# Performance work log

Measured on AMD Instinct MI355X. Metric: run time of the kernel, lower is better.

Reference implementation:

```python
import jax, jax.numpy as jnp
import numpy as np

N = 50000
E = 800000
IN_DIM = 128
OUT_DIM = 64
NEG_SLOPE = 0.2


def setup_inputs() -> dict:
    key = jax.random.key(0)
    k1, k2, k3, k4, k5 = jax.random.split(key, 5)
    X = jax.random.normal(k1, (N, IN_DIM), dtype=jnp.float32)
    edge_index = jax.random.randint(k2, (2, E), 0, N, dtype=jnp.int64)
    # parameters (xavier-ish scale)
    W = jax.random.normal(k3, (OUT_DIM, IN_DIM), dtype=jnp.float32) * (1.0 / np.sqrt(IN_DIM))
    a_src = jax.random.normal(k4, (OUT_DIM,), dtype=jnp.float32) * 0.1
    a_dst = jax.random.normal(k5, (OUT_DIM,), dtype=jnp.float32) * 0.1
    return {"X": X, "edge_index": edge_index, "num_nodes": N, "W": W, "a_src": a_src, "a_dst": a_dst}


def reference(X, edge_index, num_nodes, W, a_src, a_dst):
    H = X @ W.T                                   # [N, out_dim]
    src, dst = edge_index[0], edge_index[1]       # [E], [E]
    Hs = H[src]                                   # [E, out_dim]
    e = Hs @ a_src + H[dst] @ a_dst               # [E]
    e = jnp.where(e >= 0, e, NEG_SLOPE * e)       # leaky_relu
    e = e - jnp.max(e)                            # global max-shift (as in source)
    exp_e = jnp.exp(e)
    denom = jax.ops.segment_sum(exp_e, dst, num_segments=num_nodes)  # [N]
    alpha = exp_e / (denom[dst] + 1e-12)          # [E]
    weighted = Hs * alpha[:, None]                # [E, out_dim]
    out = jax.ops.segment_sum(weighted, dst, num_segments=num_nodes)  # [N, out_dim]
    return out
```

## Files before the change

### kernel.cpp

```cpp
#include <hip/hip_runtime.h>


#define N_NODES 50000
#define N_EDGES 800000
#define IN_DIM  128
#define OUT_DIM 64
#define NEG_SLOPE 0.2f
#define CAP       64
#define SHARD_W   6250
#define SHRD_BLKS 3200
#define SHRD_EPB  2048

#define WS_H      0
#define WS_SSRC   (N_NODES * OUT_DIM)
#define WS_SDST   (WS_SSRC + N_NODES)
#define WS_COUNT  (WS_SDST + N_NODES)
#define WS_CSR16  (WS_COUNT + N_NODES)

__device__ __forceinline__ int eidx(const void* ei, int use64, long long i) {
    return use64 ? (int)((const long long*)ei)[i] : ((const int*)ei)[i];
}

__global__ __launch_bounds__(256) void gemm_kernel(
        const float* __restrict__ X, const float* __restrict__ W,
        const float* __restrict__ a_src, const float* __restrict__ a_dst,
        float* __restrict__ H, float* __restrict__ s_src, float* __restrict__ s_dst,
        int* __restrict__ count) {
    __shared__ float sWt[IN_DIM][OUT_DIM];
    __shared__ float sX[64][76];
    const int t = threadIdx.x;
    const int row0 = blockIdx.x * 64;
    const int cg = t & 15;
    const int rg = t >> 4;

    if (t < 64 && row0 + t < N_NODES) count[row0 + t] = 0;

    for (int i = t; i < 64 * 32; i += 256) {
        int col = i & 63, k4 = i >> 6;
        float4 w = reinterpret_cast<const float4*>(W)[col * 32 + k4];
        sWt[4 * k4 + 0][col] = w.x;
        sWt[4 * k4 + 1][col] = w.y;
        sWt[4 * k4 + 2][col] = w.z;
        sWt[4 * k4 + 3][col] = w.w;
    }

    float acc[4][4];
    #pragma unroll
    for (int i = 0; i < 4; ++i)
        #pragma unroll
        for (int j = 0; j < 4; ++j) acc[i][j] = 0.f;

    #pragma unroll
    for (int kk = 0; kk < 2; ++kk) {
        const int kb = kk * 64;
        __syncthreads();
        for (int i = t; i < 64 * 16; i += 256) {
            int k4 = i & 15, row = i >> 4;
            int grow = row0 + row;
            float4 x = make_float4(0.f, 0.f, 0.f, 0.f);
            if (grow < N_NODES)
                x = reinterpret_cast<const float4*>(X)[(size_t)grow * 32 + (kb >> 2) + k4];
            sX[4 * k4 + 0][row] = x.x;
            sX[4 * k4 + 1][row] = x.y;
            sX[4 * k4 + 2][row] = x.z;
            sX[4 * k4 + 3][row] = x.w;
        }
        __syncthreads();
        #pragma unroll 4
        for (int k = 0; k < 64; ++k) {
            float4 wv = *reinterpret_cast<const float4*>(&sWt[kb + k][cg * 4]);
            float4 xv = *reinterpret_cast<const float4*>(&sX[k][rg * 4]);
            acc[0][0] += xv.x * wv.x; acc[0][1] += xv.x * wv.y;
            acc[0][2] += xv.x * wv.z; acc[0][3] += xv.x * wv.w;
            acc[1][0] += xv.y * wv.x; acc[1][1] += xv.y * wv.y;
            acc[1][2] += xv.y * wv.z; acc[1][3] += xv.y * wv.w;
            acc[2][0] += xv.z * wv.x; acc[2][1] += xv.z * wv.y;
            acc[2][2] += xv.z * wv.z; acc[2][3] += xv.z * wv.w;
            acc[3][0] += xv.w * wv.x; acc[3][1] += xv.w * wv.y;
            acc[3][2] += xv.w * wv.z; acc[3][3] += xv.w * wv.w;
        }
    }

    float4 as = *reinterpret_cast<const float4*>(&a_src[cg * 4]);
    float4 ad = *reinterpret_cast<const float4*>(&a_dst[cg * 4]);
    #pragma unroll
    for (int i = 0; i < 4; ++i) {
        float ps = acc[i][0] * as.x + acc[i][1] * as.y + acc[i][2] * as.z + acc[i][3] * as.w;
        float pd = acc[i][0] * ad.x + acc[i][1] * ad.y + acc[i][2] * ad.z + acc[i][3] * ad.w;
        #pragma unroll
        for (int off = 1; off < 16; off <<= 1) {
            ps += __shfl_xor(ps, off);
            pd += __shfl_xor(pd, off);
        }
        int row = row0 + rg * 4 + i;
        if (row < N_NODES) {
            *reinterpret_cast<float4*>(&H[(size_t)row * OUT_DIM + cg * 4]) =
                make_float4(acc[i][0], acc[i][1], acc[i][2], acc[i][3]);
            if (cg == 0) { s_src[row] = ps; s_dst[row] = pd; }
        }
    }
}

__global__ __launch_bounds__(256) void scatterfill_kernel(
        const void* __restrict__ ei, int* __restrict__ count,
        unsigned short* __restrict__ csr16) {
    __shared__ int s_use64;
    if (threadIdx.x < 64) {
        unsigned int v = ((const unsigned int*)ei)[2 * threadIdx.x + 1];
        unsigned long long nz = __ballot(v != 0u);
        if (threadIdx.x == 0) s_use64 = (nz == 0ULL) ? 1 : 0;
    }
    __syncthreads();
    const int use64 = s_use64;
    const int shard = blockIdx.x & 7;
    const int bslot = blockIdx.x >> 3;
    const unsigned int dlo = shard * SHARD_W;
    const int base = bslot * SHRD_EPB;
    for (int j = 0; j < SHRD_EPB / 256; ++j) {
        int i = base + j * 256 + threadIdx.x;
        if (i < N_EDGES) {
            unsigned int d = (unsigned int)eidx(ei, use64, (long long)N_EDGES + i);
            if (d - dlo < SHARD_W) {
                int s = eidx(ei, use64, i);
                int pos = atomicAdd(&count[d], 1);
                if (pos < CAP) csr16[((size_t)d << 6) + pos] = (unsigned short)s;
            }
        }
    }
}

__global__ __launch_bounds__(256) void aggregate_kernel(
        const float* __restrict__ H, const float* __restrict__ s_src,
        const float* __restrict__ s_dst, const int* __restrict__ count,
        const unsigned short* __restrict__ csr16, float* __restrict__ out) {
    const int lane = threadIdx.x & 63;
    const int eo   = lane >> 4;
    const int cg   = lane & 15;
    const int dst  = blockIdx.x * 4 + (threadIdx.x >> 6);
    int deg = count[dst];
    deg = (deg < CAP) ? deg : CAP;
    const size_t rs = (size_t)dst << 6;
    const float sd = s_dst[dst];

    int   sl = 0;
    float wl = 0.f;
    if (lane < deg) {
        sl = csr16[rs + lane];
        float tv = s_src[sl] + sd;
        tv = (tv >= 0.f) ? tv : NEG_SLOPE * tv;
        wl = expf(tv);
    }
    float denom = wl;
    #pragma unroll
    for (int off = 32; off; off >>= 1) denom += __shfl_xor(denom, off);

    float4 acc = make_float4(0.f, 0.f, 0.f, 0.f);
    for (int j = 0; j < deg; j += 8) {
        int ja = j + eo, jb = j + 4 + eo;
        float wa = __shfl(wl, ja);
        int   sa = __shfl(sl, ja);
        float wb = __shfl(wl, jb);
        int   sb = __shfl(sl, jb);
        if (ja >= deg) wa = 0.f;
        if (jb >= deg) wb = 0.f;
        float4 ha = *reinterpret_cast<const float4*>(&H[(size_t)sa * OUT_DIM + cg * 4]);
        float4 hb = *reinterpret_cast<const float4*>(&H[(size_t)sb * OUT_DIM + cg * 4]);
        acc.x += wa * ha.x + wb * hb.x;
        acc.y += wa * ha.y + wb * hb.y;
        acc.z += wa * ha.z + wb * hb.z;
        acc.w += wa * ha.w + wb * hb.w;
    }

    acc.x += __shfl_xor(acc.x, 16); acc.y += __shfl_xor(acc.y, 16);
    acc.z += __shfl_xor(acc.z, 16); acc.w += __shfl_xor(acc.w, 16);
    acc.x += __shfl_xor(acc.x, 32); acc.y += __shfl_xor(acc.y, 32);
    acc.z += __shfl_xor(acc.z, 32); acc.w += __shfl_xor(acc.w, 32);
    if (eo == 0) {
        float inv = 1.f / (denom + 1e-12f);
        *reinterpret_cast<float4*>(&out[(size_t)dst * OUT_DIM + cg * 4]) =
            make_float4(acc.x * inv, acc.y * inv, acc.z * inv, acc.w * inv);
    }
}

extern "C" void kernel_launch(void* const* d_in, const int* in_sizes, int n_in,
                              void* d_out, int out_size, void* d_ws, size_t ws_size,
                              hipStream_t stream) {
    const float* X     = (const float*)d_in[0];
    const void*  ei    = d_in[1];
    const float* W     = (const float*)d_in[3];
    const float* a_src = (const float*)d_in[4];
    const float* a_dst = (const float*)d_in[5];
    float* out = (float*)d_out;

    float* ws      = (float*)d_ws;
    float* H       = ws + WS_H;
    float* s_src   = ws + WS_SSRC;
    float* s_dst   = ws + WS_SDST;
    int*   count   = (int*)(ws + WS_COUNT);
    unsigned short* csr16 = (unsigned short*)(ws + WS_CSR16);

    gemm_kernel<<<(N_NODES + 63) / 64, 256, 0, stream>>>(X, W, a_src, a_dst, H, s_src, s_dst, count);
    scatterfill_kernel<<<SHRD_BLKS, 256, 0, stream>>>(ei, count, csr16);
    aggregate_kernel<<<N_NODES / 4, 256, 0, stream>>>(H, s_src, s_dst, count, csr16, out);
}
```

Before: 171.1 us.

## Merge GEMM and edge scatter-fill into one interleaved kernel launch

Combines the projection GEMM and the CSR scatter-fill into a single launch, giving one of every five blocks GEMM work and the other four scatter-fill work, so the compute-bound and atomic-bound phases can run at the same time. The count array is now zeroed by a separate memset because the GEMM blocks no longer order that reset ahead of the atomics. The GEMM stages W in 32-wide K chunks to cut shared memory and raise occupancy for the co-resident scatter blocks. In exchange it adds a memset launch and reloads W four times per GEMM block.

```diff
diff --git a/kernel.cpp b/kernel.cpp
--- a/kernel.cpp
+++ b/kernel.cpp
@@ -8,8 +8,10 @@
 #define NEG_SLOPE 0.2f
 #define CAP       64
 #define SHARD_W   6250
-#define SHRD_BLKS 3200
-#define SHRD_EPB  2048
+#define SF_BLKS   3200
+#define SF_EPB    2048
+#define GEMM_BLKS 782
+#define MERGED_BLKS 4000
 
 #define WS_H      0
 #define WS_SSRC   (N_NODES * OUT_DIM)
@@ -21,28 +23,50 @@
     return use64 ? (int)((const long long*)ei)[i] : ((const int*)ei)[i];
 }
 
-__global__ __launch_bounds__(256) void gemm_kernel(
+__global__ __launch_bounds__(256) void merged_kernel(
         const float* __restrict__ X, const float* __restrict__ W,
         const float* __restrict__ a_src, const float* __restrict__ a_dst,
+        const void* __restrict__ ei,
         float* __restrict__ H, float* __restrict__ s_src, float* __restrict__ s_dst,
-        int* __restrict__ count) {
-    __shared__ float sWt[IN_DIM][OUT_DIM];
-    __shared__ float sX[64][76];
+        int* __restrict__ count, unsigned short* __restrict__ csr16) {
+    __shared__ float sWt[32][OUT_DIM];
+    __shared__ float sX[32][76];
     const int t = threadIdx.x;
-    const int row0 = blockIdx.x * 64;
+    const unsigned int bid = blockIdx.x;
+
+    if (bid % 5 != 0) {
+        const int sf_id = bid - bid / 5 - 1;
+        __shared__ int s_use64;
+        if (t < 64) {
+            unsigned int v = ((const unsigned int*)ei)[2 * t + 1];
+            unsigned long long nz = __ballot(v != 0u);
+            if (t == 0) s_use64 = (nz == 0ULL) ? 1 : 0;
+        }
+        __syncthreads();
+        const int use64 = s_use64;
+        const int shard = sf_id & 7;
+        const int bslot = sf_id >> 3;
+        const unsigned int dlo = shard * SHARD_W;
+        const int base = bslot * SF_EPB;
+        for (int j = 0; j < SF_EPB / 256; ++j) {
+            int i = base + j * 256 + t;
+            if (i < N_EDGES) {
+                unsigned int d = (unsigned int)eidx(ei, use64, (long long)N_EDGES + i);
+                if (d - dlo < SHARD_W) {
+                    int s = eidx(ei, use64, i);
+                    int pos = atomicAdd(&count[d], 1);
+                    if (pos < CAP) csr16[((size_t)d << 6) + pos] = (unsigned short)s;
+                }
+            }
+        }
+        return;
+    }
+
+    const int gid = bid / 5;
+    if (gid >= GEMM_BLKS) return;
+    const int row0 = gid * 64;
     const int cg = t & 15;
     const int rg = t >> 4;
-
-    if (t < 64 && row0 + t < N_NODES) count[row0 + t] = 0;
-
-    for (int i = t; i < 64 * 32; i += 256) {
-        int col = i & 63, k4 = i >> 6;
-        float4 w = reinterpret_cast<const float4*>(W)[col * 32 + k4];
-        sWt[4 * k4 + 0][col] = w.x;
-        sWt[4 * k4 + 1][col] = w.y;
-        sWt[4 * k4 + 2][col] = w.z;
-        sWt[4 * k4 + 3][col] = w.w;
-    }
 
     float acc[4][4];
     #pragma unroll
@@ -51,24 +75,32 @@
         for (int j = 0; j < 4; ++j) acc[i][j] = 0.f;
 
     #pragma unroll
-    for (int kk = 0; kk < 2; ++kk) {
-        const int kb = kk * 64;
+    for (int c = 0; c < 4; ++c) {
+        const int kb = c * 32;
         __syncthreads();
-        for (int i = t; i < 64 * 16; i += 256) {
-            int k4 = i & 15, row = i >> 4;
+        for (int i = t; i < 512; i += 256) {
+            int col = i & 63, q = i >> 6;
+            float4 w = reinterpret_cast<const float4*>(W)[col * 32 + (kb >> 2) + q];
+            sWt[4 * q + 0][col] = w.x;
+            sWt[4 * q + 1][col] = w.y;
+            sWt[4 * q + 2][col] = w.z;
+            sWt[4 * q + 3][col] = w.w;
+        }
+        for (int i = t; i < 512; i += 256) {
+            int q = i & 7, row = i >> 3;
             int grow = row0 + row;
             float4 x = make_float4(0.f, 0.f, 0.f, 0.f);
             if (grow < N_NODES)
-                x = reinterpret_cast<const float4*>(X)[(size_t)grow * 32 + (kb >> 2) + k4];
-            sX[4 * k4 + 0][row] = x.x;
-            sX[4 * k4 + 1][row] = x.y;
-            sX[4 * k4 + 2][row] = x.z;
-            sX[4 * k4 + 3][row] = x.w;
+                x = reinterpret_cast<const float4*>(X)[(size_t)grow * 32 + (kb >> 2) + q];
+            sX[4 * q + 0][row] = x.x;
+            sX[4 * q + 1][row] = x.y;
+            sX[4 * q + 2][row] = x.z;
+            sX[4 * q + 3][row] = x.w;
         }
         __syncthreads();
         #pragma unroll 4
-        for (int k = 0; k < 64; ++k) {
-            float4 wv = *reinterpret_cast<const float4*>(&sWt[kb + k][cg * 4]);
+        for (int k = 0; k < 32; ++k) {
+            float4 wv = *reinterpret_cast<const float4*>(&sWt[k][cg * 4]);
             float4 xv = *reinterpret_cast<const float4*>(&sX[k][rg * 4]);
             acc[0][0] += xv.x * wv.x; acc[0][1] += xv.x * wv.y;
             acc[0][2] += xv.x * wv.z; acc[0][3] += xv.x * wv.w;
@@ -97,34 +129,6 @@
             *reinterpret_cast<float4*>(&H[(size_t)row * OUT_DIM + cg * 4]) =
                 make_float4(acc[i][0], acc[i][1], acc[i][2], acc[i][3]);
             if (cg == 0) { s_src[row] = ps; s_dst[row] = pd; }
-        }
-    }
-}
-
-__global__ __launch_bounds__(256) void scatterfill_kernel(
-        const void* __restrict__ ei, int* __restrict__ count,
-        unsigned short* __restrict__ csr16) {
-    __shared__ int s_use64;
-    if (threadIdx.x < 64) {
-        unsigned int v = ((const unsigned int*)ei)[2 * threadIdx.x + 1];
-        unsigned long long nz = __ballot(v != 0u);
-        if (threadIdx.x == 0) s_use64 = (nz == 0ULL) ? 1 : 0;
-    }
-    __syncthreads();
-    const int use64 = s_use64;
-    const int shard = blockIdx.x & 7;
-    const int bslot = blockIdx.x >> 3;
-    const unsigned int dlo = shard * SHARD_W;
-    const int base = bslot * SHRD_EPB;
-    for (int j = 0; j < SHRD_EPB / 256; ++j) {
-        int i = base + j * 256 + threadIdx.x;
-        if (i < N_EDGES) {
-            unsigned int d = (unsigned int)eidx(ei, use64, (long long)N_EDGES + i);
-            if (d - dlo < SHARD_W) {
-                int s = eidx(ei, use64, i);
-                int pos = atomicAdd(&count[d], 1);
-                if (pos < CAP) csr16[((size_t)d << 6) + pos] = (unsigned short)s;
-            }
         }
     }
 }
@@ -199,7 +203,8 @@
     int*   count   = (int*)(ws + WS_COUNT);
     unsigned short* csr16 = (unsigned short*)(ws + WS_CSR16);
 
-    gemm_kernel<<<(N_NODES + 63) / 64, 256, 0, stream>>>(X, W, a_src, a_dst, H, s_src, s_dst, count);
-    scatterfill_kernel<<<SHRD_BLKS, 256, 0, stream>>>(ei, count, csr16);
+    hipMemsetAsync(count, 0, (size_t)N_NODES * sizeof(int), stream);
+    merged_kernel<<<MERGED_BLKS, 256, 0, stream>>>(X, W, a_src, a_dst, ei,
+                                                   H, s_src, s_dst, count, csr16);
     aggregate_kernel<<<N_NODES / 4, 256, 0, stream>>>(H, s_src, s_dst, count, csr16, out);
 }
```

New measurement: 155.4 us. 1.1x faster.
